# Kernel tuning notes

Measured on AMD Instinct MI355X. Metric: run time of the kernel, lower is better.

## Reference

```python
import jax, jax.numpy as jnp
import numpy as np

N_HEAD = 16
EPS = 1e-6


def setup_inputs() -> dict:
    key = jax.random.key(0)
    k1, k2, k3 = jax.random.split(key, 3)
    B, T, C = 2, 2048, 1024
    x = jax.random.normal(k1, (B, T, C), dtype=jnp.float32)
    w_attn = jax.random.normal(k2, (C, 3 * C), dtype=jnp.float32) * 0.02
    w_proj = jax.random.normal(k3, (C, C), dtype=jnp.float32) * 0.02
    return {"x": x, "w_attn": w_attn, "w_proj": w_proj}


def _linear_attention(q, k, v):
    """q,k,v: (T,B,H,D) with q,k already feature-mapped (elu+1).
    Causal linear attention via a D x D running-state recurrence (same math
    as cumsum of k-v outer products, computed without the O(T*D^2) tensor)."""
    B, H, D = q.shape[1], q.shape[2], q.shape[3]

    def step(carry, qkv_t):
        S, z = carry                      # S:(B,H,D,D), z:(B,H,D)
        qt, kt, vt = qkv_t                # each (B,H,D)
        S = S + kt[..., :, None] * vt[..., None, :]
        z = z + kt
        num = jnp.einsum('bhi,bhij->bhj', qt, S)
        den = jnp.sum(qt * z, axis=-1, keepdims=True)
        return (S, z), num / (den + EPS)

    S0 = jnp.zeros((B, H, D, D), q.dtype)
    z0 = jnp.zeros((B, H, D), q.dtype)
    _, y = jax.lax.scan(step, (S0, z0), (q, k, v))
    return y                              # (T,B,H,D)


def reference(x, w_attn, w_proj):
    B, T, C = x.shape
    H = N_HEAD
    D = C // H
    qkv = x @ w_attn                      # (B,T,3C)
    q, k, v = jnp.split(qkv, 3, axis=-1)

    def to_tbhd(a):                       # (B,T,C) -> (T,B,H,D)
        return a.reshape(B, T, H, D).transpose(1, 0, 2, 3)

    q = jax.nn.elu(to_tbhd(q)) + 1.0      # phi(x) = ELU(x)+1
    k = jax.nn.elu(to_tbhd(k)) + 1.0
    v = to_tbhd(v)

    y = _linear_attention(q, k, v)        # (T,B,H,D)
    y = y.transpose(1, 0, 2, 3).reshape(B, T, C)
    return y @ w_proj                     # resid dropout p=0.0 is identity
```

## Files before the change

kernel.cpp:

```cpp
#include <hip/hip_runtime.h>
#include <hip/hip_bf16.h>
#include <cmath>

#define TB   2048
#define CCH  1024
#define NCH  32
#define EPSF 1e-6f

typedef unsigned short u16;
typedef __attribute__((ext_vector_type(8))) short  frag8;
typedef __attribute__((ext_vector_type(4))) float  floatx4;

__device__ __forceinline__ u16 f2bf(float f) {
    unsigned int u = __float_as_uint(f);
    unsigned int r = (u + 0x7fffu + ((u >> 16) & 1u)) >> 16;
    return (u16)r;
}
__device__ __forceinline__ float bf2f(u16 v) {
    return __uint_as_float(((unsigned int)v) << 16);
}

__device__ __forceinline__ void async_load16(const u16* g, u16* l) {
    __builtin_amdgcn_global_load_lds(
        (const __attribute__((address_space(1))) void*)g,
        (__attribute__((address_space(3))) void*)l,
        16, 0, 0);
}

__global__ __launch_bounds__(256) void prep_k(
    const float* __restrict__ x, const float* __restrict__ wa,
    const float* __restrict__ wp,
    u16* __restrict__ xb, u16* __restrict__ waT, u16* __restrict__ wpT)
{
    __shared__ u16 t[64][72];
    int blk = blockIdx.x;
    if (blk < 2048) {
        int i = (blk * 256 + threadIdx.x) * 8;
        float4 a = *(const float4*)(x + i);
        float4 b = *(const float4*)(x + i + 4);
        u16 v[8];
        v[0] = f2bf(a.x); v[1] = f2bf(a.y); v[2] = f2bf(a.z); v[3] = f2bf(a.w);
        v[4] = f2bf(b.x); v[5] = f2bf(b.y); v[6] = f2bf(b.z); v[7] = f2bf(b.w);
        *(uint4*)(xb + i) = *(uint4*)v;
        return;
    }
    const float* in; u16* out; int K, N, bx, by;
    if (blk < 2048 + 768) {
        int tb = blk - 2048; in = wa; out = waT; K = 1024; N = 3072;
        bx = tb % 48; by = tb / 48;
    } else {
        int tb = blk - 2816; in = wp; out = wpT; K = 1024; N = 1024;
        bx = tb & 15; by = tb >> 4;
    }
    const int k0 = by * 64, n0 = bx * 64;
    #pragma unroll
    for (int i = 0; i < 4; ++i) {
        int rr = (threadIdx.x >> 4) + 16 * i;
        int c4 = (threadIdx.x & 15) * 4;
        float4 v = *(const float4*)(in + (size_t)(k0 + rr) * N + n0 + c4);
        t[c4 + 0][rr] = f2bf(v.x);
        t[c4 + 1][rr] = f2bf(v.y);
        t[c4 + 2][rr] = f2bf(v.z);
        t[c4 + 3][rr] = f2bf(v.w);
    }
    __syncthreads();
    #pragma unroll
    for (int i = 0; i < 2; ++i) {
        int rr = (threadIdx.x >> 3) + 32 * i;
        int c8 = (threadIdx.x & 7) * 8;
        u16 o[8];
        #pragma unroll
        for (int q = 0; q < 8; ++q) o[q] = t[rr][c8 + q];
        *(uint4*)(out + (size_t)(n0 + rr) * K + k0 + c8) = *(uint4*)o;
    }
}

#define PHASE(P, STAGE_STMT, VMW) do {                                        \
    frag8 af[4][2], bf[2][2];                                                 \
    _Pragma("unroll")                                                         \
    for (int m = 0; m < 4; ++m)                                               \
      _Pragma("unroll")                                                       \
      for (int kk = 0; kk < 2; ++kk)                                          \
        af[m][kk] = *(const frag8*)&Abuf[(P) >= 4][(((P) >> 1) & 1) * 8192    \
            + (wm * 64 + m * 16 + lrow) * 64 + (((kk * 4 + quad) ^ rsw) * 8)];\
    _Pragma("unroll")                                                         \
    for (int n = 0; n < 2; ++n)                                               \
      _Pragma("unroll")                                                       \
      for (int kk = 0; kk < 2; ++kk)                                          \
        bf[n][kk] = *(const frag8*)&Bbuf[(P) >= 4][((P) & 1) * 8192           \
            + (wn * 32 + n * 16 + lrow) * 64 + (((kk * 4 + quad) ^ rsw) * 8)];\
    STAGE_STMT;                                                               \
    __builtin_amdgcn_sched_barrier(0);                                        \
    if (VMW) asm volatile("s_waitcnt vmcnt(4)" ::: "memory");                 \
    __builtin_amdgcn_s_barrier();                                             \
    __builtin_amdgcn_sched_barrier(0);                                        \
    __builtin_amdgcn_s_setprio(1);                                            \
    _Pragma("unroll")                                                         \
    for (int m = 0; m < 4; ++m)                                               \
      _Pragma("unroll")                                                       \
      for (int n = 0; n < 2; ++n)                                             \
        _Pragma("unroll")                                                     \
        for (int kk = 0; kk < 2; ++kk)                                        \
          acc[(((P) >> 1) & 1) * 4 + m][((P) & 1) * 2 + n] =                  \
            __builtin_amdgcn_mfma_f32_16x16x32_bf16(                          \
              af[m][kk], bf[n][kk],                                           \
              acc[(((P) >> 1) & 1) * 4 + m][((P) & 1) * 2 + n], 0, 0, 0);     \
    __builtin_amdgcn_s_setprio(0);                                            \
    __builtin_amdgcn_sched_barrier(0);                                        \
    __builtin_amdgcn_s_barrier();                                             \
  } while (0)

__global__ __launch_bounds__(512, 2) void gemm1_256_k(
    const u16* __restrict__ Ag, const u16* __restrict__ BTg,
    u16* __restrict__ Cg, int N, int K, int phi_cols)
{
    __shared__ u16 Abuf[2][16384];
    __shared__ u16 Bbuf[2][16384];
    const int tid  = threadIdx.x;
    const int wave = tid >> 6, lane = tid & 63;
    const int quad = lane >> 4, lrow = lane & 15;
    const int wm = wave >> 2, wn = wave & 3;
    const int lr = lane >> 3;
    const int lc = ((lane & 7) ^ lr) * 8;
    const int rsw = lrow & 7;
    const int NKT = K >> 6;

    int bid = blockIdx.x;
    int swz = (bid & 7) * 24 + (bid >> 3);
    int by = swz / 12, bx = swz - by * 12;
    const int row0 = by * 256, col0 = bx * 256;

    floatx4 acc[8][4] = {};

    auto stageA = [&](int kt, int hh) {
        int ktc = kt < NKT ? kt : NKT - 1;
        u16* dst = &Abuf[ktc & 1][hh * 8192];
        #pragma unroll
        for (int m2 = 0; m2 < 2; ++m2) {
            int i = wave * 2 + m2;
            int lrid = i * 8 + lr;
            int grow = row0 + (lrid & 63) + hh * 64 + ((lrid >> 6) << 7);
            async_load16(Ag + (size_t)grow * K + ktc * 64 + lc, dst + i * 512);
        }
    };
    auto stageB = [&](int kt, int hh) {
        int ktc = kt < NKT ? kt : NKT - 1;
        u16* dst = &Bbuf[ktc & 1][hh * 8192];
        #pragma unroll
        for (int m2 = 0; m2 < 2; ++m2) {
            int i = wave * 2 + m2;
            int lrid = i * 8 + lr;
            int gcol = col0 + (lrid & 31) + hh * 32 + ((lrid >> 5) << 6);
            async_load16(BTg + (size_t)gcol * K + ktc * 64 + lc, dst + i * 512);
        }
    };

    stageA(0, 0); stageB(0, 0); stageA(0, 1); stageB(0, 1);
    stageA(1, 0); stageB(1, 0);
    __builtin_amdgcn_sched_barrier(0);
    asm volatile("s_waitcnt vmcnt(4)" ::: "memory");
    __builtin_amdgcn_s_barrier();
    __builtin_amdgcn_sched_barrier(0);

    for (int it = 0; it < (NKT >> 1); ++it) {
        const int ka = it * 2, kb = ka + 1;
        PHASE(0, stageA(kb, 1),     false);
        PHASE(1, stageB(kb, 1),     false);
        PHASE(2, stageA(ka + 2, 0), false);
        PHASE(3, stageB(ka + 2, 0), true);
        PHASE(4, stageA(ka + 2, 1), false);
        PHASE(5, stageB(ka + 2, 1), false);
        PHASE(6, stageA(kb + 2, 0), false);
        PHASE(7, stageB(kb + 2, 0), true);
    }

    #pragma unroll
    for (int M = 0; M < 8; ++M) {
        #pragma unroll
        for (int NN = 0; NN < 4; ++NN) {
            int col = col0 + wn * 64 + (NN >> 1) * 32 + (NN & 1) * 16 + lrow;
            bool isphi = col < phi_cols;
            #pragma unroll
            for (int r = 0; r < 4; ++r) {
                int row = row0 + wm * 128 + (M >> 2) * 64 + (M & 3) * 16 + quad * 4 + r;
                float v = acc[M][NN][r];
                if (isphi) v = (v > 0.f) ? (v + 1.f) : __expf(v);
                Cg[(size_t)row * N + col] = f2bf(v);
            }
        }
    }
}

__global__ __launch_bounds__(256) void gemm_bf16_f32out_k(
    const u16* __restrict__ A, const u16* __restrict__ BT,
    float* __restrict__ C, int N, int K)
{
    __shared__ u16 Als[128 * 128];
    __shared__ u16 Bls[64 * 128];
    const int tid  = threadIdx.x;
    const int wave = tid >> 6, lane = tid & 63;
    const int quad = lane >> 4, lrow = lane & 15;
    const int wm = wave >> 1, wn = wave & 1;
    const int row0 = blockIdx.y * 128, col0 = blockIdx.x * 64;
    const int lr4 = lane >> 4;
    floatx4 acc[4][2] = {};

    for (int k0 = 0; k0 < K; k0 += 128) {
        __syncthreads();
        #pragma unroll
        for (int m = 0; m < 8; ++m) {
            int rbase = wave * 32 + m * 4;
            int cg = (lane & 15) ^ ((rbase + lr4) & 15);
            async_load16(A + (size_t)(row0 + rbase + lr4) * K + k0 + cg * 8,
                         &Als[rbase * 128]);
        }
        #pragma unroll
        for (int m = 0; m < 4; ++m) {
            int rbase = wave * 16 + m * 4;
            int cg = (lane & 15) ^ ((rbase + lr4) & 15);
            async_load16(BT + (size_t)(col0 + rbase + lr4) * K + k0 + cg * 8,
                         &Bls[rbase * 128]);
        }
        __syncthreads();
        #pragma unroll
        for (int ksi = 0; ksi < 4; ++ksi) {
            frag8 af[4], bf[2];
            #pragma unroll
            for (int i = 0; i < 4; ++i)
                af[i] = *(const frag8*)&Als[(wm * 64 + i * 16 + lrow) * 128
                                            + ((ksi * 4 + quad) ^ lrow) * 8];
            #pragma unroll
            for (int jn = 0; jn < 2; ++jn)
                bf[jn] = *(const frag8*)&Bls[(wn * 32 + jn * 16 + lrow) * 128
                                             + ((ksi * 4 + quad) ^ lrow) * 8];
            #pragma unroll
            for (int i = 0; i < 4; ++i)
                #pragma unroll
                for (int jn = 0; jn < 2; ++jn)
                    acc[i][jn] = __builtin_amdgcn_mfma_f32_16x16x32_bf16(
                        af[i], bf[jn], acc[i][jn], 0, 0, 0);
        }
    }

    #pragma unroll
    for (int i = 0; i < 4; ++i)
        #pragma unroll
        for (int jn = 0; jn < 2; ++jn) {
            int col = col0 + wn * 32 + jn * 16 + lrow;
            #pragma unroll
            for (int r = 0; r < 4; ++r) {
                int row = row0 + wm * 64 + i * 16 + quad * 4 + r;
                C[(size_t)row * N + col] = acc[i][jn][r];
            }
        }
}

__global__ __launch_bounds__(256) void chunk_kv_mfma_k(
    const u16* __restrict__ qkv,
    u16* __restrict__ Spt,
    float* __restrict__ zloc,
    u16* __restrict__ VtG)
{
    __shared__ u16 Kt[64][72];
    __shared__ u16 Vt[64][72];
    const int tid  = threadIdx.x;
    const int wave = tid >> 6, lane = tid & 63;
    const int quad = lane >> 4, lrow = lane & 15;
    const int blk = blockIdx.x;
    const int c = blk & 31, h = (blk >> 5) & 15, b = blk >> 9;
    const int t0 = c * 64;
    const u16* base = qkv + (size_t)(b * TB + t0) * 3072 + h * 64;

    #pragma unroll
    for (int m = 0; m < 2; ++m) {
        int chunk = tid + 256 * m;
        int s = chunk >> 3, d0 = (chunk & 7) * 8;
        const u16* row = base + (size_t)s * 3072;
        u16 kv[8], vv[8];
        *(uint4*)kv = *(const uint4*)(row + 1024 + d0);
        *(uint4*)vv = *(const uint4*)(row + 2048 + d0);
        #pragma unroll
        for (int q = 0; q < 8; ++q) { Kt[d0 + q][s] = kv[q]; Vt[d0 + q][s] = vv[q]; }
    }
    __syncthreads();

    #pragma unroll
    for (int m = 0; m < 2; ++m) {
        int e = tid + 256 * m;
        int r = e >> 3, c8 = (e & 7) * 8;
        u16 o[8];
        #pragma unroll
        for (int q = 0; q < 8; ++q) o[q] = Vt[r][c8 + q];
        *(uint4*)(VtG + (size_t)blk * 4096 + r * 64 + c8) = *(uint4*)o;
    }

    frag8 vf[2];
    #pragma unroll
    for (int ks = 0; ks < 2; ++ks)
        vf[ks] = *(const frag8*)&Vt[wave * 16 + lrow][ks * 32 + quad * 8];
    u16* So = Spt + (size_t)blk * 4096;
    #pragma unroll
    for (int jn = 0; jn < 4; ++jn) {
        floatx4 acc = {};
        #pragma unroll
        for (int ks = 0; ks < 2; ++ks) {
            frag8 kf = *(const frag8*)&Kt[jn * 16 + lrow][ks * 32 + quad * 8];
            acc = __builtin_amdgcn_mfma_f32_16x16x32_bf16(vf[ks], kf, acc, 0, 0, 0);
        }
        #pragma unroll
        for (int r = 0; r < 4; ++r) {
            int j = wave * 16 + quad * 4 + r;
            int i = jn * 16 + lrow;
            So[j * 64 + i] = f2bf(acc[r]);
        }
    }
    if (tid < 64) {
        float z = 0.f;
        for (int s = 0; s < 64; ++s) z += bf2f(Kt[tid][s]);
        zloc[(size_t)blk * 64 + tid] = z;
    }
}

__global__ __launch_bounds__(256) void scan_state_k(
    u16* __restrict__ Spt, float* __restrict__ z)
{
    const int bh = blockIdx.x >> 1;
    const int part = blockIdx.x & 1;
    const int e0 = part * 2048 + threadIdx.x * 8;
    const size_t base = (size_t)bh * NCH * 4096;
    float r[8] = {};
    for (int c = 0; c < NCH; ++c) {
        u16* p = Spt + base + (size_t)c * 4096 + e0;
        u16 t[8];
        *(uint4*)t = *(const uint4*)p;
        u16 o[8];
        #pragma unroll
        for (int q = 0; q < 8; ++q) { o[q] = f2bf(r[q]); r[q] += bf2f(t[q]); }
        *(uint4*)p = *(uint4*)o;
    }
    if (part == 0 && threadIdx.x < 64) {
        const size_t zb = (size_t)bh * NCH * 64;
        float rz = 0.f;
        for (int c = 0; c < NCH; ++c) {
            float t = z[zb + c * 64 + threadIdx.x];
            z[zb + c * 64 + threadIdx.x] = rz;
            rz += t;
        }
    }
}

__global__ __launch_bounds__(256) void attn_mfma_k(
    const u16* __restrict__ qkv,
    const u16* __restrict__ SptG,
    const float* __restrict__ zp,
    const u16* __restrict__ VtG,
    u16* __restrict__ Yb)
{
    __shared__ u16 Qls[64 * 64];
    __shared__ u16 Kls[64 * 64];
    __shared__ u16 Vls[64 * 64];
    __shared__ u16 Sls[64 * 64];
    __shared__ float zps[64];
    __shared__ float den4[64][4];
    __shared__ float den[64];

    const int tid  = threadIdx.x;
    const int wave = tid >> 6, lane = tid & 63;
    const int quad = lane >> 4, lrow = lane & 15;
    const int blk = blockIdx.x;
    const int c = blk & 31, h = (blk >> 5) & 15, b = blk >> 9;
    const int t0 = c * 64;
    const int lr = lane >> 3;
    const int lc = ((lane & 7) ^ lr) * 8;
    const int rsw = lrow & 7;
    const u16* qbase = qkv + (size_t)(b * TB + t0) * 3072 + h * 64;

    #pragma unroll
    for (int m = 0; m < 2; ++m) {
        int i = wave * 2 + m;
        int r = i * 8 + lr;
        async_load16(qbase + (size_t)r * 3072 + lc,          &Qls[i * 512]);
        async_load16(qbase + (size_t)r * 3072 + 1024 + lc,   &Kls[i * 512]);
        async_load16(SptG + (size_t)blk * 4096 + r * 64 + lc, &Sls[i * 512]);
        async_load16(VtG  + (size_t)blk * 4096 + r * 64 + lc, &Vls[i * 512]);
    }
    if (tid < 64) zps[tid] = zp[(size_t)blk * 64 + tid];
    __syncthreads();

    frag8 qf[2];
    #pragma unroll
    for (int ks = 0; ks < 2; ++ks)
        qf[ks] = *(const frag8*)&Qls[(wave * 16 + lrow) * 64 + ((ks * 4 + quad) ^ rsw) * 8];

    floatx4 yacc[4] = {}, kacc[4] = {};
    #pragma unroll
    for (int jn = 0; jn < 4; ++jn) {
        #pragma unroll
        for (int ks = 0; ks < 2; ++ks) {
            frag8 spf = *(const frag8*)&Sls[(jn * 16 + lrow) * 64 + ((ks * 4 + quad) ^ rsw) * 8];
            yacc[jn] = __builtin_amdgcn_mfma_f32_16x16x32_bf16(qf[ks], spf, yacc[jn], 0, 0, 0);
            frag8 kf = *(const frag8*)&Kls[(jn * 16 + lrow) * 64 + ((ks * 4 + quad) ^ rsw) * 8];
            kacc[jn] = __builtin_amdgcn_mfma_f32_16x16x32_bf16(qf[ks], kf, kacc[jn], 0, 0, 0);
        }
    }
    __syncthreads();

    #pragma unroll
    for (int jn = 0; jn < 4; ++jn) {
        int s = jn * 16 + lrow;
        #pragma unroll
        for (int r = 0; r < 4; ++r) {
            int t = wave * 16 + quad * 4 + r;
            float v = (s <= t) ? kacc[jn][r] : 0.f;
            Sls[t * 64 + (((s >> 3) ^ (t & 7)) * 8) + (s & 7)] = f2bf(v);
        }
    }
    __syncthreads();

    {
        int t = tid >> 2, seg = tid & 3;
        float p = 0.f;
        #pragma unroll
        for (int g2 = 0; g2 < 2; ++g2) {
            int g = seg * 2 + g2;
            int pq = ((g ^ (t & 7)) * 8);
            const u16* qp = &Qls[t * 64 + pq];
            const u16* ap = &Sls[t * 64 + pq];
            #pragma unroll
            for (int e = 0; e < 8; ++e) {
                p += bf2f(qp[e]) * zps[g * 8 + e] + bf2f(ap[e]);
            }
        }
        den4[t][seg] = p;
    }

    frag8 af2[2];
    #pragma unroll
    for (int ks = 0; ks < 2; ++ks)
        af2[ks] = *(const frag8*)&Sls[(wave * 16 + lrow) * 64 + ((ks * 4 + quad) ^ rsw) * 8];
    #pragma unroll
    for (int jn = 0; jn < 4; ++jn)
        #pragma unroll
        for (int ks = 0; ks < 2; ++ks) {
            frag8 vf = *(const frag8*)&Vls[(jn * 16 + lrow) * 64 + ((ks * 4 + quad) ^ rsw) * 8];
            yacc[jn] = __builtin_amdgcn_mfma_f32_16x16x32_bf16(af2[ks], vf, yacc[jn], 0, 0, 0);
        }
    __syncthreads();
    if (tid < 64) den[tid] = den4[tid][0] + den4[tid][1] + den4[tid][2] + den4[tid][3];
    __syncthreads();

    #pragma unroll
    for (int jn = 0; jn < 4; ++jn) {
        #pragma unroll
        for (int r = 0; r < 4; ++r) {
            int t = wave * 16 + quad * 4 + r;
            float inv = 1.f / (den[t] + EPSF);
            Qls[t * 64 + jn * 16 + lrow] = f2bf(yacc[jn][r] * inv);
        }
    }
    __syncthreads();
    {
        int row = tid >> 2, seg = tid & 3;
        size_t o = (size_t)(b * TB + t0 + row) * CCH + h * 64 + seg * 16;
        *(uint4*)(Yb + o)     = *(uint4*)&Qls[row * 64 + seg * 16];
        *(uint4*)(Yb + o + 8) = *(uint4*)&Qls[row * 64 + seg * 16 + 8];
    }
}

extern "C" void kernel_launch(void* const* d_in, const int* in_sizes, int n_in,
                              void* d_out, int out_size, void* d_ws, size_t ws_size,
                              hipStream_t stream)
{
    const float* x      = (const float*)d_in[0];
    const float* w_attn = (const float*)d_in[1];
    const float* w_proj = (const float*)d_in[2];
    float* out = (float*)d_out;

    u16* xb    = (u16*)d_ws;
    u16* waT   = xb    + (size_t)4096 * 1024;
    u16* wpT   = waT   + (size_t)3072 * 1024;
    u16* Yb    = wpT   + (size_t)1024 * 1024;
    u16* qkv_b = Yb    + (size_t)4096 * 1024;
    u16* Spt   = qkv_b + (size_t)4096 * 3072;
    u16* VtG   = Spt   + (size_t)1024 * 4096;
    float* zloc = (float*)(VtG + (size_t)1024 * 4096);

    prep_k<<<3072, 256, 0, stream>>>(x, w_attn, w_proj, xb, waT, wpT);

    gemm1_256_k<<<192, 512, 0, stream>>>(xb, waT, qkv_b, 3072, 1024, 2048);

    chunk_kv_mfma_k<<<1024, 256, 0, stream>>>(qkv_b, Spt, zloc, VtG);
    scan_state_k   <<<64,   256, 0, stream>>>(Spt, zloc);
    attn_mfma_k    <<<1024, 256, 0, stream>>>(qkv_b, Spt, zloc, VtG, Yb);

    gemm_bf16_f32out_k<<<dim3(16, 32), 256, 0, stream>>>(Yb, wpT, out, 1024, 1024);
}
```

Measured before the change: 169.9 us.

## Reorder GEMM1 phases to reuse A/B fragments and deepen load prefetch

Restructures the QKV GEMM main loop so each K tile runs its four quadrant products in a snake order (00, 01, 11, 10). This lets loaded A and B register fragments be reused across consecutive phases instead of reloading both from LDS every phase. The prefetch schedule changes to keep more async global loads in flight, waiting with vmcnt(12) before every phase. The loop count is hardcoded to 8 iterations (K=1024), which ties the kernel to that shape, and the deeper prefetch adds risk to LDS buffer hazards.

```diff
diff --git a/kernel.cpp b/kernel.cpp
--- a/kernel.cpp
+++ b/kernel.cpp
@@ -75,47 +75,39 @@
     }
 }
 
-#define PHASE(P, STAGE_STMT, VMW) do {                                        \
-    frag8 af[4][2], bf[2][2];                                                 \
-    _Pragma("unroll")                                                         \
-    for (int m = 0; m < 4; ++m)                                               \
-      _Pragma("unroll")                                                       \
-      for (int kk = 0; kk < 2; ++kk)                                          \
-        af[m][kk] = *(const frag8*)&Abuf[(P) >= 4][(((P) >> 1) & 1) * 8192    \
-            + (wm * 64 + m * 16 + lrow) * 64 + (((kk * 4 + quad) ^ rsw) * 8)];\
-    _Pragma("unroll")                                                         \
-    for (int n = 0; n < 2; ++n)                                               \
-      _Pragma("unroll")                                                       \
-      for (int kk = 0; kk < 2; ++kk)                                          \
-        bf[n][kk] = *(const frag8*)&Bbuf[(P) >= 4][((P) & 1) * 8192           \
-            + (wn * 32 + n * 16 + lrow) * 64 + (((kk * 4 + quad) ^ rsw) * 8)];\
-    STAGE_STMT;                                                               \
-    __builtin_amdgcn_sched_barrier(0);                                        \
-    if (VMW) asm volatile("s_waitcnt vmcnt(4)" ::: "memory");                 \
-    __builtin_amdgcn_s_barrier();                                             \
-    __builtin_amdgcn_sched_barrier(0);                                        \
+#define RD_A(MH, BUF) do {                                                    \
+    _Pragma("unroll") for (int m = 0; m < 4; ++m)                             \
+      _Pragma("unroll") for (int kk = 0; kk < 2; ++kk)                        \
+        af[m][kk] = *(const frag8*)&Asm[(BUF)*16384 + (MH)*8192               \
+            + (wm*64 + m*16 + lrow)*64 + (((kk*4+quad)^rsw)*8)];              \
+  } while(0)
+#define RD_B(NH, BUF, DST) do {                                               \
+    _Pragma("unroll") for (int n = 0; n < 2; ++n)                             \
+      _Pragma("unroll") for (int kk = 0; kk < 2; ++kk)                        \
+        DST[n][kk] = *(const frag8*)&Bsm[(BUF)*16384 + (NH)*8192              \
+            + (wn*32 + n*16 + lrow)*64 + (((kk*4+quad)^rsw)*8)];              \
+  } while(0)
+#define MM(MH, NH, BF) do {                                                   \
     __builtin_amdgcn_s_setprio(1);                                            \
-    _Pragma("unroll")                                                         \
-    for (int m = 0; m < 4; ++m)                                               \
-      _Pragma("unroll")                                                       \
-      for (int n = 0; n < 2; ++n)                                             \
-        _Pragma("unroll")                                                     \
-        for (int kk = 0; kk < 2; ++kk)                                        \
-          acc[(((P) >> 1) & 1) * 4 + m][((P) & 1) * 2 + n] =                  \
-            __builtin_amdgcn_mfma_f32_16x16x32_bf16(                          \
-              af[m][kk], bf[n][kk],                                           \
-              acc[(((P) >> 1) & 1) * 4 + m][((P) & 1) * 2 + n], 0, 0, 0);     \
+    _Pragma("unroll") for (int m = 0; m < 4; ++m)                             \
+      _Pragma("unroll") for (int n = 0; n < 2; ++n)                           \
+        _Pragma("unroll") for (int kk = 0; kk < 2; ++kk)                      \
+          acc[(MH)*4+m][(NH)*2+n] = __builtin_amdgcn_mfma_f32_16x16x32_bf16(  \
+              af[m][kk], BF[n][kk], acc[(MH)*4+m][(NH)*2+n], 0, 0, 0);        \
     __builtin_amdgcn_s_setprio(0);                                            \
-    __builtin_amdgcn_sched_barrier(0);                                        \
-    __builtin_amdgcn_s_barrier();                                             \
-  } while (0)
+  } while(0)
+#define SYNC_PRE() do { __builtin_amdgcn_sched_barrier(0);                    \
+    asm volatile("s_waitcnt vmcnt(12)" ::: "memory");                         \
+    __builtin_amdgcn_s_barrier(); __builtin_amdgcn_sched_barrier(0); } while(0)
+#define SYNC_POST() do { __builtin_amdgcn_sched_barrier(0);                   \
+    __builtin_amdgcn_s_barrier(); } while(0)
 
 __global__ __launch_bounds__(512, 2) void gemm1_256_k(
     const u16* __restrict__ Ag, const u16* __restrict__ BTg,
     u16* __restrict__ Cg, int N, int K, int phi_cols)
 {
-    __shared__ u16 Abuf[2][16384];
-    __shared__ u16 Bbuf[2][16384];
+    __shared__ u16 Asm[2 * 16384];
+    __shared__ u16 Bsm[2 * 16384];
     const int tid  = threadIdx.x;
     const int wave = tid >> 6, lane = tid & 63;
     const int quad = lane >> 4, lrow = lane & 15;
@@ -131,47 +123,55 @@
     const int row0 = by * 256, col0 = bx * 256;
 
     floatx4 acc[8][4] = {};
-
-    auto stageA = [&](int kt, int hh) {
-        int ktc = kt < NKT ? kt : NKT - 1;
-        u16* dst = &Abuf[ktc & 1][hh * 8192];
-        #pragma unroll
-        for (int m2 = 0; m2 < 2; ++m2) {
-            int i = wave * 2 + m2;
-            int lrid = i * 8 + lr;
-            int grow = row0 + (lrid & 63) + hh * 64 + ((lrid >> 6) << 7);
-            async_load16(Ag + (size_t)grow * K + ktc * 64 + lc, dst + i * 512);
+    frag8 af[4][2], bf0[2][2], bf1[2][2];
+
+    auto stage = [&](int tile, int kind) {
+        if (tile > NKT - 1) tile = NKT - 1;
+        const int buf = tile & 1;
+        if (kind == 0 || kind == 3) {
+            const int hh = (kind == 3);
+            u16* dst = Asm + buf * 16384 + hh * 8192;
+            #pragma unroll
+            for (int m2 = 0; m2 < 2; ++m2) {
+                int i = wave * 2 + m2;
+                int lrid = i * 8 + lr;
+                int grow = row0 + (lrid & 63) + hh * 64 + ((lrid >> 6) << 7);
+                async_load16(Ag + (size_t)grow * K + tile * 64 + lc, dst + i * 512);
+            }
+        } else {
+            const int hh = (kind == 2);
+            u16* dst = Bsm + buf * 16384 + hh * 8192;
+            #pragma unroll
+            for (int m2 = 0; m2 < 2; ++m2) {
+                int i = wave * 2 + m2;
+                int lrid = i * 8 + lr;
+                int gcol = col0 + (lrid & 31) + hh * 32 + ((lrid >> 5) << 6);
+                async_load16(BTg + (size_t)gcol * K + tile * 64 + lc, dst + i * 512);
+            }
         }
     };
-    auto stageB = [&](int kt, int hh) {
-        int ktc = kt < NKT ? kt : NKT - 1;
-        u16* dst = &Bbuf[ktc & 1][hh * 8192];
-        #pragma unroll
-        for (int m2 = 0; m2 < 2; ++m2) {
-            int i = wave * 2 + m2;
-            int lrid = i * 8 + lr;
-            int gcol = col0 + (lrid & 31) + hh * 32 + ((lrid >> 5) << 6);
-            async_load16(BTg + (size_t)gcol * K + ktc * 64 + lc, dst + i * 512);
-        }
-    };
-
-    stageA(0, 0); stageB(0, 0); stageA(0, 1); stageB(0, 1);
-    stageA(1, 0); stageB(1, 0);
-    __builtin_amdgcn_sched_barrier(0);
-    asm volatile("s_waitcnt vmcnt(4)" ::: "memory");
-    __builtin_amdgcn_s_barrier();
-    __builtin_amdgcn_sched_barrier(0);
-
-    for (int it = 0; it < (NKT >> 1); ++it) {
+
+    stage(0, 0); stage(0, 1); stage(0, 2); stage(0, 3);
+    stage(1, 0); stage(1, 1); stage(1, 2);
+
+    for (int it = 0; it < 8; ++it) {
         const int ka = it * 2, kb = ka + 1;
-        PHASE(0, stageA(kb, 1),     false);
-        PHASE(1, stageB(kb, 1),     false);
-        PHASE(2, stageA(ka + 2, 0), false);
-        PHASE(3, stageB(ka + 2, 0), true);
-        PHASE(4, stageA(ka + 2, 1), false);
-        PHASE(5, stageB(ka + 2, 1), false);
-        PHASE(6, stageA(kb + 2, 0), false);
-        PHASE(7, stageB(kb + 2, 0), true);
+        RD_A(0, 0); RD_B(0, 0, bf0); stage(kb, 3);
+        SYNC_PRE(); MM(0, 0, bf0); SYNC_POST();
+        RD_B(1, 0, bf1); stage(ka + 2, 0);
+        SYNC_PRE(); MM(0, 1, bf1); SYNC_POST();
+        RD_A(1, 0); stage(ka + 2, 1);
+        SYNC_PRE(); MM(1, 1, bf1); SYNC_POST();
+        stage(ka + 2, 2);
+        SYNC_PRE(); MM(1, 0, bf0); SYNC_POST();
+        RD_A(0, 1); RD_B(0, 1, bf0); stage(ka + 2, 3);
+        SYNC_PRE(); MM(0, 0, bf0); SYNC_POST();
+        RD_B(1, 1, bf1); stage(kb + 2, 0);
+        SYNC_PRE(); MM(0, 1, bf1); SYNC_POST();
+        RD_A(1, 1); stage(kb + 2, 1);
+        SYNC_PRE(); MM(1, 1, bf1); SYNC_POST();
+        stage(kb + 2, 2);
+        SYNC_PRE(); MM(1, 0, bf0); SYNC_POST();
     }
 
     #pragma unroll
```

Result: faster. 163.3 us (-3.9%).
